# Performance work log

Measured on AMD Instinct MI355X. Metric: run time of the kernel, lower is better.

Reference implementation:

```python
import jax, jax.numpy as jnp
import numpy as np

B, F, H, D, K = 16384, 4096, 512, 64, 512  # batch, feat, hidden, emb_dim, codebook size
M = H // D  # code positions per sample


def _leaky(h):
    return jnp.where(h > 0, h, 0.01 * h)


def setup_inputs() -> dict:
    key = jax.random.key(0)
    ks = jax.random.split(key, 16)
    lin = lambda k, i, o: jax.random.normal(k, (i, o), jnp.float32) * (1.0 / np.sqrt(i))
    return {
        "x": jax.random.uniform(ks[0], (B, F), jnp.float32),
        "We1": lin(ks[1], F, 256), "be1": jnp.zeros((256,), jnp.float32),
        "We2": lin(ks[2], 256, 128), "be2": jnp.zeros((128,), jnp.float32),
        "We3": lin(ks[3], 128, H), "be3": jnp.zeros((H,), jnp.float32),
        "Wd1": lin(ks[4], H, 128), "bd1": jnp.zeros((128,), jnp.float32),
        "Wd2": lin(ks[5], 128, 256), "bd2": jnp.zeros((256,), jnp.float32),
        "Wd3": lin(ks[6], 256, F), "bd3": jnp.zeros((F,), jnp.float32),
        "codebook": jax.random.normal(ks[7], (D, K), jnp.float32) * 0.02,  # (emb_dim, num_embeddings)
    }


def _nearest(z_e, codebook):
    # z_e: (B, D, M); codebook: (D, K). Squared-distance argmin over K.
    x2 = jnp.sum(z_e * z_e, axis=1)                       # (B, M)
    xw = jnp.einsum('bdm,dk->bmk', z_e, codebook)         # (B, M, K)
    w2 = jnp.sum(codebook * codebook, axis=0)             # (K,)
    idx = jnp.argmin(x2[..., None] - 2.0 * xw + w2, axis=-1)  # (B, M)
    quant = jnp.swapaxes(codebook.T[idx], 1, 2)           # (B, D, M)
    return quant, idx


def reference(x, We1, be1, We2, be2, We3, be3, Wd1, bd1, Wd2, bd2, Wd3, bd3, codebook):
    # encoder MLP
    h = _leaky(x @ We1 + be1)
    h = _leaky(h @ We2 + be2)
    h = _leaky(h @ We3 + be3)                             # (B, H)
    z_e = h.reshape(B, D, M)
    # emb(z_e, weight_sg=True): straight-through, weight detached
    quant_sg, idx = _nearest(z_e, jax.lax.stop_gradient(codebook))
    z_q = z_e + jax.lax.stop_gradient(quant_sg - z_e)
    # emb(z_e.detach()): grads (if any) flow to codebook via gather
    emb, _ = _nearest(jax.lax.stop_gradient(z_e), codebook)
    # decoder MLP
    g = _leaky(z_q.reshape(B, H) @ Wd1 + bd1)
    g = _leaky(g @ Wd2 + bd2)
    X_pred = jax.nn.sigmoid(g @ Wd3 + bd3)                # (B, F)
    return idx, z_e, z_q, emb, X_pred
```

## Files before the change

### kernel.cpp

```cpp
#include <hip/hip_runtime.h>
#include <cstdint>
#include <cstddef>


static constexpr int BB = 16384;
static constexpr int TM = 128, TN = 128, TK = 16;

typedef __attribute__((ext_vector_type(8))) short short8;
typedef __attribute__((ext_vector_type(8))) _Float16 half8;
typedef __attribute__((ext_vector_type(4))) float f32x4;

__device__ __forceinline__ unsigned short f2bf(float f) {
    union { float f; uint32_t u; } v; v.f = f;
    uint32_t r = (v.u + 0x7FFFu + ((v.u >> 16) & 1u)) >> 16;
    return (unsigned short)r;
}

__device__ __forceinline__ int bsw(int c) { return c + ((c >> 5) << 2); }

#define GLL16(gp, lp) \
    __builtin_amdgcn_global_load_lds( \
        (const __attribute__((address_space(1))) uint32_t*)(gp), \
        (__attribute__((address_space(3))) uint32_t*)(lp), 16, 0, 0)

__global__ __launch_bounds__(256) void gemm_fp32(
    const float* __restrict__ A, const float* __restrict__ Bm,
    const float* __restrict__ bias, float* __restrict__ C,
    float* __restrict__ part,
    int M, int N, int Kd, int kLen, int act)
{
    __shared__ float As[TK][TM + 4];
    __shared__ float Bs[TK][140];
    const int tid = threadIdx.x;
    const int bm = blockIdx.y * TM;
    const int bn = blockIdx.x * TN;
    const int kStart = blockIdx.z * kLen;
    const int tx = tid & 15;
    const int ty = tid >> 4;

    const int arow = tid >> 2;
    const int acol = (tid & 3) << 2;
    const int brow = tid >> 5;
    const int bcol = (tid & 31) << 2;

    float acc[8][8];
#pragma unroll
    for (int i = 0; i < 8; i++)
#pragma unroll
        for (int j = 0; j < 8; j++) acc[i][j] = 0.f;

    const float* Ap0 = A + (size_t)(bm + arow) * Kd + acol;
    const float* Ap1 = A + (size_t)(bm + arow + 64) * Kd + acol;
    const float* Bp0 = Bm + (size_t)brow * N + bn + bcol;
    const float* Bp1 = Bm + (size_t)(brow + 8) * N + bn + bcol;

    const int pb0 = bsw(bcol);
    const int prb0 = bsw(tx * 8);
    const int prb1 = prb0 + 4;

    for (int k0 = kStart; k0 < kStart + kLen; k0 += TK) {
        const float4 a0 = *(const float4*)(Ap0 + k0);
        const float4 a1 = *(const float4*)(Ap1 + k0);
        const float4 b0 = *(const float4*)(Bp0 + (size_t)k0 * N);
        const float4 b1 = *(const float4*)(Bp1 + (size_t)k0 * N);
        __syncthreads();
        As[acol + 0][arow] = a0.x; As[acol + 1][arow] = a0.y;
        As[acol + 2][arow] = a0.z; As[acol + 3][arow] = a0.w;
        As[acol + 0][arow + 64] = a1.x; As[acol + 1][arow + 64] = a1.y;
        As[acol + 2][arow + 64] = a1.z; As[acol + 3][arow + 64] = a1.w;
        *(float4*)&Bs[brow][pb0]     = b0;
        *(float4*)&Bs[brow + 8][pb0] = b1;
        __syncthreads();
#pragma unroll
        for (int kk = 0; kk < TK; kk++) {
            float a[8], b[8];
            *(float4*)&a[0] = *(const float4*)&As[kk][ty * 8];
            *(float4*)&a[4] = *(const float4*)&As[kk][ty * 8 + 4];
            *(float4*)&b[0] = *(const float4*)&Bs[kk][prb0];
            *(float4*)&b[4] = *(const float4*)&Bs[kk][prb1];
#pragma unroll
            for (int i = 0; i < 8; i++)
#pragma unroll
                for (int j = 0; j < 8; j++)
                    acc[i][j] = fmaf(a[i], b[j], acc[i][j]);
        }
    }

    if (part) {
        float* P = part + (size_t)blockIdx.z * M * N;
#pragma unroll
        for (int i = 0; i < 8; i++) {
            const int row = bm + ty * 8 + i;
            *(float4*)&P[(size_t)row * N + bn + tx * 8]     = *(float4*)&acc[i][0];
            *(float4*)&P[(size_t)row * N + bn + tx * 8 + 4] = *(float4*)&acc[i][4];
        }
        return;
    }

    float bv[8];
#pragma unroll
    for (int j = 0; j < 8; j++) bv[j] = bias[bn + tx * 8 + j];
#pragma unroll
    for (int i = 0; i < 8; i++) {
        const int row = bm + ty * 8 + i;
        float o[8];
#pragma unroll
        for (int j = 0; j < 8; j++) {
            float v = acc[i][j] + bv[j];
            if (act == 0) v = (v > 0.f) ? v : 0.01f * v;
            else          v = 1.0f / (1.0f + __expf(-v));
            o[j] = v;
        }
        *(float4*)&C[(size_t)row * N + bn + tx * 8]     = *(float4*)&o[0];
        *(float4*)&C[(size_t)row * N + bn + tx * 8 + 4] = *(float4*)&o[4];
    }
}

__global__ __launch_bounds__(256) void combine_act(
    const float* __restrict__ part, int S, size_t MN,
    const float* __restrict__ bias, int N,
    float* __restrict__ outF, unsigned short* __restrict__ outB)
{
    const size_t e = ((size_t)blockIdx.x * 256 + threadIdx.x) * 4;
    if (e >= MN) return;
    float4 s = *(const float4*)(part + e);
    for (int i = 1; i < S; i++) {
        const float4 p = *(const float4*)(part + (size_t)i * MN + e);
        s.x += p.x; s.y += p.y; s.z += p.z; s.w += p.w;
    }
    const int col = (int)(e & (size_t)(N - 1));
    const float4 bv = *(const float4*)(bias + col);
    float v0 = s.x + bv.x, v1 = s.y + bv.y, v2 = s.z + bv.z, v3 = s.w + bv.w;
    v0 = (v0 > 0.f) ? v0 : 0.01f * v0;
    v1 = (v1 > 0.f) ? v1 : 0.01f * v1;
    v2 = (v2 > 0.f) ? v2 : 0.01f * v2;
    v3 = (v3 > 0.f) ? v3 : 0.01f * v3;
    if (outF) {
        float4 o; o.x = v0; o.y = v1; o.z = v2; o.w = v3;
        *(float4*)(outF + e) = o;
    } else {
        ushort4 o; o.x = f2bf(v0); o.y = f2bf(v1); o.z = f2bf(v2); o.w = f2bf(v3);
        *(ushort4*)(outB + e) = o;
    }
}

__global__ __launch_bounds__(256) void transpose_cast(
    const float* __restrict__ W, unsigned short* __restrict__ WT, int R, int Cc)
{
    __shared__ float s[32][33];
    const int tx = threadIdx.x & 31, ty = threadIdx.x >> 5;
    const int c0 = blockIdx.x * 32, r0 = blockIdx.y * 32;
#pragma unroll
    for (int i = 0; i < 4; i++)
        s[ty + i * 8][tx] = W[(size_t)(r0 + ty + i * 8) * Cc + c0 + tx];
    __syncthreads();
#pragma unroll
    for (int i = 0; i < 4; i++)
        WT[(size_t)(c0 + ty + i * 8) * R + r0 + tx] = f2bf(s[tx][ty + i * 8]);
}

__global__ __launch_bounds__(256) void transpose_split_f16(
    const float* __restrict__ W, unsigned short* __restrict__ Th,
    unsigned short* __restrict__ Tl, int R, int Cc)
{
    __shared__ float s[32][33];
    const int tx = threadIdx.x & 31, ty = threadIdx.x >> 5;
    const int c0 = blockIdx.x * 32, r0 = blockIdx.y * 32;
#pragma unroll
    for (int i = 0; i < 4; i++)
        s[ty + i * 8][tx] = W[(size_t)(r0 + ty + i * 8) * Cc + c0 + tx];
    __syncthreads();
#pragma unroll
    for (int i = 0; i < 4; i++) {
        const float f = s[tx][ty + i * 8];
        const _Float16 h = (_Float16)f;
        const float fh = (float)h;
        const _Float16 lo = (_Float16)((f - fh) * 4096.0f);
        union { _Float16 hf; unsigned short u; } ch, cl;
        ch.hf = h; cl.hf = lo;
        Th[(size_t)(c0 + ty + i * 8) * R + r0 + tx] = ch.u;
        Tl[(size_t)(c0 + ty + i * 8) * R + r0 + tx] = cl.u;
    }
}

__global__ __launch_bounds__(256, 2) void gemm_f16x2_enc1(
    const float* __restrict__ X,
    const unsigned short* __restrict__ Bh,
    const unsigned short* __restrict__ Bl,
    float* __restrict__ part)
{
    __shared__ short Ah[2][2048];
    __shared__ short Al[2][2048];
    const int tid = threadIdx.x;
    const int l = tid & 63, w = tid >> 6;
    const int lm = l & 15, lq = l >> 4;
    const int bm = blockIdx.y * 64;
    const int kStart = blockIdx.z * 2048;

    const float* gA = X + (size_t)(bm + w * 16 + lm) * 4096 + kStart + lq * 8;
    const unsigned short* gBh = Bh + (size_t)(w * 64 + lm) * 4096 + kStart + lq * 8;
    const unsigned short* gBl = Bl + (size_t)(w * 64 + lm) * 4096 + kStart + lq * 8;
    const size_t rstep = (size_t)16 * 4096;

    const int aoff = (w << 9) + (l << 3);
    const int fr0 = (lq << 7) + (lm << 3);

    f32x4 acc1[4][4], acc2[4][4];
#pragma unroll
    for (int i = 0; i < 4; i++)
#pragma unroll
        for (int j = 0; j < 4; j++) {
            acc1[i][j] = (f32x4){0.f, 0.f, 0.f, 0.f};
            acc2[i][j] = (f32x4){0.f, 0.f, 0.f, 0.f};
        }

    {
        float fv[8];
        *(f32x4*)&fv[0] = __builtin_nontemporal_load((const f32x4*)(gA));
        *(f32x4*)&fv[4] = __builtin_nontemporal_load((const f32x4*)(gA + 4));
        union { _Float16 h[8]; short8 s; } uh, ul;
#pragma unroll
        for (int e = 0; e < 8; e++) {
            const float f = fv[e];
            const _Float16 h = (_Float16)f;
            const float fh = (float)h;
            uh.h[e] = h;
            ul.h[e] = (_Float16)((f - fh) * 4096.0f);
        }
        *(short8*)&Ah[0][aoff] = uh.s;
        *(short8*)&Al[0][aoff] = ul.s;
    }

    for (int k0 = 0; k0 < 2048; k0 += 32) {
        const int buf = (k0 >> 5) & 1;
        const int nb = buf ^ 1;
        const int kn = k0 + 32;
        __syncthreads();
        half8 bh[4], bl[4];
#pragma unroll
        for (int j = 0; j < 4; j++) {
            bh[j] = *(const half8*)(gBh + (size_t)j * rstep + k0);
            bl[j] = *(const half8*)(gBl + (size_t)j * rstep + k0);
        }
        f32x4 a0, a1;
        if (kn < 2048) {
            a0 = __builtin_nontemporal_load((const f32x4*)(gA + kn));
            a1 = __builtin_nontemporal_load((const f32x4*)(gA + kn + 4));
        }
        half8 ah[4];
#pragma unroll
        for (int i = 0; i < 4; i++)
            ah[i] = *(const half8*)&Ah[buf][(i << 9) + fr0];
#pragma unroll
        for (int i = 0; i < 4; i++)
#pragma unroll
            for (int j = 0; j < 4; j++)
                acc1[i][j] = __builtin_amdgcn_mfma_f32_16x16x32_f16(
                    ah[i], bh[j], acc1[i][j], 0, 0, 0);
#pragma unroll
        for (int i = 0; i < 4; i++)
#pragma unroll
            for (int j = 0; j < 4; j++)
                acc2[i][j] = __builtin_amdgcn_mfma_f32_16x16x32_f16(
                    ah[i], bl[j], acc2[i][j], 0, 0, 0);
        half8 al[4];
#pragma unroll
        for (int i = 0; i < 4; i++)
            al[i] = *(const half8*)&Al[buf][(i << 9) + fr0];
#pragma unroll
        for (int i = 0; i < 4; i++)
#pragma unroll
            for (int j = 0; j < 4; j++)
                acc2[i][j] = __builtin_amdgcn_mfma_f32_16x16x32_f16(
                    al[i], bh[j], acc2[i][j], 0, 0, 0);
        if (kn < 2048) {
            float fv[8];
            *(f32x4*)&fv[0] = a0;
            *(f32x4*)&fv[4] = a1;
            union { _Float16 h[8]; short8 s; } uh, ul;
#pragma unroll
            for (int e = 0; e < 8; e++) {
                const float f = fv[e];
                const _Float16 h = (_Float16)f;
                const float fh = (float)h;
                uh.h[e] = h;
                ul.h[e] = (_Float16)((f - fh) * 4096.0f);
            }
            *(short8*)&Ah[nb][aoff] = uh.s;
            *(short8*)&Al[nb][aoff] = ul.s;
        }
    }

    float* P = part + (size_t)blockIdx.z * BB * 256;
    const float inv = 0.000244140625f;
#pragma unroll
    for (int i = 0; i < 4; i++)
#pragma unroll
        for (int j = 0; j < 4; j++) {
            const int col = w * 64 + j * 16 + lm;
#pragma unroll
            for (int r = 0; r < 4; r++) {
                const int row = bm + i * 16 + lq * 4 + r;
                P[(size_t)row * 256 + col] = acc1[i][j][r] + inv * acc2[i][j][r];
            }
        }
}

__global__ __launch_bounds__(256) void gemm_bf16_dec3(
    const unsigned short* __restrict__ Ag,
    const unsigned short* __restrict__ Bt,
    const float* __restrict__ bias, float* __restrict__ C)
{
    __shared__ short As[4096];
    __shared__ short Bs2[4096];
    const int tid = threadIdx.x;
    const int l = tid & 63, w = tid >> 6;
    const int lm = l & 15, lq = l >> 4;
    const int bm = blockIdx.y * 128, bn = blockIdx.x * 128;
    const int wm = (w >> 1) * 64, wn = (w & 1) * 64;

    const int t0 = w * 2, t1 = w * 2 + 1;
    const unsigned short* ga0 = Ag + (size_t)(bm + t0 * 16 + lm) * 256 + lq * 8;
    const unsigned short* ga1 = Ag + (size_t)(bm + t1 * 16 + lm) * 256 + lq * 8;
    const unsigned short* gb0 = Bt + (size_t)(bn + t0 * 16 + lm) * 256 + lq * 8;
    const unsigned short* gb1 = Bt + (size_t)(bn + t1 * 16 + lm) * 256 + lq * 8;

    f32x4 acc[4][4];
#pragma unroll
    for (int i = 0; i < 4; i++)
#pragma unroll
        for (int j = 0; j < 4; j++) acc[i][j] = (f32x4){0.f, 0.f, 0.f, 0.f};

    for (int k0 = 0; k0 < 256; k0 += 32) {
        __syncthreads();
        GLL16(ga0 + k0, &As[t0 * 512]);
        GLL16(ga1 + k0, &As[t1 * 512]);
        GLL16(gb0 + k0, &Bs2[t0 * 512]);
        GLL16(gb1 + k0, &Bs2[t1 * 512]);
        __syncthreads();
        short8 af[4], bf[4];
#pragma unroll
        for (int i = 0; i < 4; i++)
            af[i] = *(const short8*)&As[((w >> 1) * 4 + i) * 512 + lq * 128 + lm * 8];
#pragma unroll
        for (int j = 0; j < 4; j++)
            bf[j] = *(const short8*)&Bs2[((w & 1) * 4 + j) * 512 + lq * 128 + lm * 8];
#pragma unroll
        for (int i = 0; i < 4; i++)
#pragma unroll
            for (int j = 0; j < 4; j++)
                acc[i][j] = __builtin_amdgcn_mfma_f32_16x16x32_bf16(
                    af[i], bf[j], acc[i][j], 0, 0, 0);
    }

#pragma unroll
    for (int i = 0; i < 4; i++) {
#pragma unroll
        for (int j = 0; j < 4; j++) {
            const int col = bn + wn + j * 16 + lm;
            const float bv = bias[col];
#pragma unroll
            for (int r = 0; r < 4; r++) {
                const int row = bm + wm + i * 16 + lq * 4 + r;
                float v = acc[i][j][r] + bv;
                v = 1.0f / (1.0f + __expf(-v));
                C[(size_t)row * 4096 + col] = v;
            }
        }
    }
}

__global__ __launch_bounds__(512) void vq_argmin(
    const float* __restrict__ ze, const float* __restrict__ cb,
    float* __restrict__ idxf)
{
    __shared__ float cbs[64 * 512];
    __shared__ float As[64][68];
    __shared__ float w2s[512];
    const int tid = threadIdx.x;
    const int p0 = blockIdx.x * 64;

    const float4* cb4 = (const float4*)cb;
    float4* cbs4 = (float4*)cbs;
    for (int i = tid; i < 8192; i += 512) cbs4[i] = cb4[i];

    const float4* ze4 = (const float4*)(ze + (size_t)p0 * 64);
    for (int i = tid; i < 1024; i += 512) {
        float4 v = ze4[i];
        int e = i * 4;
        int bo = e >> 9, r = e & 511;
        int d = r >> 3, m = r & 7;
        *(float4*)&As[d][bo * 8 + m] = v;
    }
    __syncthreads();

    {
        float s = 0.f;
#pragma unroll
        for (int d = 0; d < 64; ++d) { float c = cbs[d * 512 + tid]; s = fmaf(c, c, s); }
        w2s[tid] = s;
    }
    __syncthreads();

    const int tx = tid & 63;
    const int ty = tid >> 6;

    float acc[8][8], x2a[8];
#pragma unroll
    for (int i = 0; i < 8; i++) {
        x2a[i] = 0.f;
#pragma unroll
        for (int j = 0; j < 8; j++) acc[i][j] = 0.f;
    }

#pragma unroll 8
    for (int kk = 0; kk < 64; ++kk) {
        float a[8], b[8];
        *(float4*)&a[0] = *(const float4*)&As[kk][ty * 8];
        *(float4*)&a[4] = *(const float4*)&As[kk][ty * 8 + 4];
        *(float4*)&b[0] = *(const float4*)&cbs[kk * 512 + tx * 8];
        *(float4*)&b[4] = *(const float4*)&cbs[kk * 512 + tx * 8 + 4];
#pragma unroll
        for (int i = 0; i < 8; i++) x2a[i] = fmaf(a[i], a[i], x2a[i]);
#pragma unroll
        for (int i = 0; i < 8; i++)
#pragma unroll
            for (int j = 0; j < 8; j++)
                acc[i][j] = fmaf(a[i], b[j], acc[i][j]);
    }

    float w2v[8];
#pragma unroll
    for (int j = 0; j < 8; j++) w2v[j] = w2s[tx * 8 + j];

#pragma unroll
    for (int i = 0; i < 8; i++) {
        float bd = 3.4e38f; int bk = 1 << 30;
#pragma unroll
        for (int j = 0; j < 8; j++) {
            float dsc = (x2a[i] - 2.0f * acc[i][j]) + w2v[j];
            if (dsc < bd) { bd = dsc; bk = tx * 8 + j; }
        }
        for (int off = 32; off > 0; off >>= 1) {
            float od = __shfl_xor(bd, off);
            int   ok = __shfl_xor(bk, off);
            if (od < bd || (od == bd && ok < bk)) { bd = od; bk = ok; }
        }
        if (tx == i) idxf[p0 + ty * 8 + i] = (float)bk;
    }
}

__global__ __launch_bounds__(256) void vq_gather(
    const float* __restrict__ ze, const float* __restrict__ idxf,
    const float* __restrict__ cb,
    float* __restrict__ zq, float* __restrict__ emb)
{
    const int t = blockIdx.x * 256 + threadIdx.x;
    const int e = t * 4;
    const int b = e >> 9, r = e & 511;
    const int d = r >> 3, m = r & 7;
    const float4 z = *(const float4*)(ze + e);
    float q[4];
#pragma unroll
    for (int c = 0; c < 4; c++) {
        int k = (int)idxf[b * 8 + m + c];
        q[c] = cb[d * 512 + k];
    }
    float4 zq4, em4;
    zq4.x = z.x + (q[0] - z.x); zq4.y = z.y + (q[1] - z.y);
    zq4.z = z.z + (q[2] - z.z); zq4.w = z.w + (q[3] - z.w);
    em4.x = q[0]; em4.y = q[1]; em4.z = q[2]; em4.w = q[3];
    *(float4*)(zq + e) = zq4;
    *(float4*)(emb + e) = em4;
}

extern "C" void kernel_launch(void* const* d_in, const int* in_sizes, int n_in,
                              void* d_out, int out_size, void* d_ws, size_t ws_size,
                              hipStream_t stream)
{
    const float* x   = (const float*)d_in[0];
    const float* We1 = (const float*)d_in[1];
    const float* be1 = (const float*)d_in[2];
    const float* We2 = (const float*)d_in[3];
    const float* be2 = (const float*)d_in[4];
    const float* We3 = (const float*)d_in[5];
    const float* be3 = (const float*)d_in[6];
    const float* Wd1 = (const float*)d_in[7];
    const float* bd1 = (const float*)d_in[8];
    const float* Wd2 = (const float*)d_in[9];
    const float* bd2 = (const float*)d_in[10];
    const float* Wd3 = (const float*)d_in[11];
    const float* bd3 = (const float*)d_in[12];
    const float* cb  = (const float*)d_in[13];

    float* out   = (float*)d_out;
    float* o_idx = out;
    float* o_ze  = o_idx + 131072;
    float* o_zq  = o_ze + 8388608;
    float* o_emb = o_zq + 8388608;
    float* o_X   = o_emb + 8388608;

    float* h1 = (float*)d_ws;
    float* h2 = h1 + (size_t)BB * 256;
    float* g1 = h1;
    unsigned short* g2b = (unsigned short*)(h1 + (size_t)BB * 128);
    unsigned short* WT  = (unsigned short*)h2;

    unsigned short* Bth = (unsigned short*)(o_X + 16777216);
    unsigned short* Btl = Bth + 1048576;

    transpose_split_f16<<<dim3(8, 128), 256, 0, stream>>>(We1, Bth, Btl, 4096, 256);
    gemm_f16x2_enc1<<<dim3(1, 256, 2), 256, 0, stream>>>(x, Bth, Btl, o_X);
    combine_act<<<4096, 256, 0, stream>>>(o_X, 2, (size_t)BB * 256, be1, 256, h1, nullptr);
    gemm_fp32<<<dim3(1, 128, 2), 256, 0, stream>>>(
        h1, We2, nullptr, nullptr, o_X, BB, 128, 256, 128, 0);
    combine_act<<<2048, 256, 0, stream>>>(o_X, 2, (size_t)BB * 128, be2, 128, h2, nullptr);
    gemm_fp32<<<dim3(4, 128, 1), 256, 0, stream>>>(
        h2, We3, be3, o_ze, nullptr, BB, 512, 128, 128, 0);

    vq_argmin<<<dim3(2048), dim3(512), 0, stream>>>(o_ze, cb, o_idx);
    vq_gather<<<dim3(8192), dim3(256), 0, stream>>>(o_ze, o_idx, cb, o_zq, o_emb);

    transpose_cast<<<dim3(128, 8), 256, 0, stream>>>(Wd3, WT, 256, 4096);

    gemm_fp32<<<dim3(1, 128, 4), 256, 0, stream>>>(
        o_zq, Wd1, nullptr, nullptr, o_X, BB, 128, 512, 128, 0);
    combine_act<<<2048, 256, 0, stream>>>(o_X, 4, (size_t)BB * 128, bd1, 128, g1, nullptr);
    gemm_fp32<<<dim3(2, 128, 2), 256, 0, stream>>>(
        g1, Wd2, nullptr, nullptr, o_X, BB, 256, 128, 64, 0);
    combine_act<<<4096, 256, 0, stream>>>(o_X, 2, (size_t)BB * 256, bd2, 256, nullptr, g2b);
    gemm_bf16_dec3<<<dim3(32, 128), 256, 0, stream>>>(g2b, WT, bd3, o_X);
}
```

Baseline: 1.080 ms.

## Deepen software pipeline in enc1 GEMM with register-prefetched B-high and two-ahead A loads

Restructures the first encoder GEMM's main loop into a templated step, unrolled by two. The B-high fragments for the next k-step are prefetched into ping-pong registers and the fp32 A tile is loaded two steps ahead, so global load latency is hidden behind more MFMA work. The cost is more live registers (an extra B buffer and the A prefetch), which may pressure the 2-blocks-per-CU launch bound or cause spills.

```diff
diff --git a/kernel.cpp b/kernel.cpp
--- a/kernel.cpp
+++ b/kernel.cpp
@@ -183,6 +183,79 @@
     }
 }
 
+template<int BUF>
+__device__ __forceinline__ void enc1_step(
+    int K0,
+    const float* __restrict__ gA,
+    const unsigned short* __restrict__ gBh,
+    const unsigned short* __restrict__ gBl,
+    short (&Ah)[2][2048], short (&Al)[2][2048],
+    half8 (&bhC)[4], half8 (&bhN)[4], half8 (&blS)[4],
+    f32x4& p0, f32x4& p1,
+    f32x4 (&acc1)[4][4], f32x4 (&acc2)[4][4],
+    int aoff, int fr0)
+{
+    constexpr size_t rstep = (size_t)16 * 4096;
+    const int kn1 = K0 + 32, kn2 = K0 + 64;
+    __syncthreads();
+#pragma unroll
+    for (int j = 0; j < 4; j++)
+        blS[j] = *(const half8*)(gBl + (size_t)j * rstep + K0);
+    if (kn1 < 2048) {
+#pragma unroll
+        for (int j = 0; j < 4; j++)
+            bhN[j] = *(const half8*)(gBh + (size_t)j * rstep + kn1);
+    }
+    f32x4 f0, f1;
+    if (kn2 < 2048) {
+        f0 = __builtin_nontemporal_load((const f32x4*)(gA + kn2));
+        f1 = __builtin_nontemporal_load((const f32x4*)(gA + kn2 + 4));
+    }
+    half8 ah[4];
+#pragma unroll
+    for (int i = 0; i < 4; i++)
+        ah[i] = *(const half8*)&Ah[BUF][(i << 9) + fr0];
+#pragma unroll
+    for (int i = 0; i < 4; i++)
+#pragma unroll
+        for (int j = 0; j < 4; j++)
+            acc1[i][j] = __builtin_amdgcn_mfma_f32_16x16x32_f16(
+                ah[i], bhC[j], acc1[i][j], 0, 0, 0);
+#pragma unroll
+    for (int i = 0; i < 4; i++)
+#pragma unroll
+        for (int j = 0; j < 4; j++)
+            acc2[i][j] = __builtin_amdgcn_mfma_f32_16x16x32_f16(
+                ah[i], blS[j], acc2[i][j], 0, 0, 0);
+    half8 al[4];
+#pragma unroll
+    for (int i = 0; i < 4; i++)
+        al[i] = *(const half8*)&Al[BUF][(i << 9) + fr0];
+#pragma unroll
+    for (int i = 0; i < 4; i++)
+#pragma unroll
+        for (int j = 0; j < 4; j++)
+            acc2[i][j] = __builtin_amdgcn_mfma_f32_16x16x32_f16(
+                al[i], bhC[j], acc2[i][j], 0, 0, 0);
+    if (kn1 < 2048) {
+        float fv[8];
+        *(f32x4*)&fv[0] = p0;
+        *(f32x4*)&fv[4] = p1;
+        union { _Float16 h[8]; short8 s; } uh, ul;
+#pragma unroll
+        for (int e = 0; e < 8; e++) {
+            const float f = fv[e];
+            const _Float16 h = (_Float16)f;
+            const float fh = (float)h;
+            uh.h[e] = h;
+            ul.h[e] = (_Float16)((f - fh) * 4096.0f);
+        }
+        *(short8*)&Ah[BUF ^ 1][aoff] = uh.s;
+        *(short8*)&Al[BUF ^ 1][aoff] = ul.s;
+    }
+    if (kn2 < 2048) { p0 = f0; p1 = f1; }
+}
+
 __global__ __launch_bounds__(256, 2) void gemm_f16x2_enc1(
     const float* __restrict__ X,
     const unsigned short* __restrict__ Bh,
@@ -200,7 +273,7 @@
     const float* gA = X + (size_t)(bm + w * 16 + lm) * 4096 + kStart + lq * 8;
     const unsigned short* gBh = Bh + (size_t)(w * 64 + lm) * 4096 + kStart + lq * 8;
     const unsigned short* gBl = Bl + (size_t)(w * 64 + lm) * 4096 + kStart + lq * 8;
-    const size_t rstep = (size_t)16 * 4096;
+    constexpr size_t rstep = (size_t)16 * 4096;
 
     const int aoff = (w << 9) + (l << 3);
     const int fr0 = (lq << 7) + (lm << 3);
@@ -214,10 +287,20 @@
             acc2[i][j] = (f32x4){0.f, 0.f, 0.f, 0.f};
         }
 
+    half8 bhA[4], bhB[4], blS[4];
+    f32x4 p0, p1;
+
     {
+#pragma unroll
+        for (int j = 0; j < 4; j++)
+            bhA[j] = *(const half8*)(gBh + (size_t)j * rstep);
+        f32x4 a0 = __builtin_nontemporal_load((const f32x4*)(gA));
+        f32x4 a1 = __builtin_nontemporal_load((const f32x4*)(gA + 4));
+        p0 = __builtin_nontemporal_load((const f32x4*)(gA + 32));
+        p1 = __builtin_nontemporal_load((const f32x4*)(gA + 36));
         float fv[8];
-        *(f32x4*)&fv[0] = __builtin_nontemporal_load((const f32x4*)(gA));
-        *(f32x4*)&fv[4] = __builtin_nontemporal_load((const f32x4*)(gA + 4));
+        *(f32x4*)&fv[0] = a0;
+        *(f32x4*)&fv[4] = a1;
         union { _Float16 h[8]; short8 s; } uh, ul;
 #pragma unroll
         for (int e = 0; e < 8; e++) {
@@ -231,64 +314,11 @@
         *(short8*)&Al[0][aoff] = ul.s;
     }
 
-    for (int k0 = 0; k0 < 2048; k0 += 32) {
-        const int buf = (k0 >> 5) & 1;
-        const int nb = buf ^ 1;
-        const int kn = k0 + 32;
-        __syncthreads();
-        half8 bh[4], bl[4];
-#pragma unroll
-        for (int j = 0; j < 4; j++) {
-            bh[j] = *(const half8*)(gBh + (size_t)j * rstep + k0);
-            bl[j] = *(const half8*)(gBl + (size_t)j * rstep + k0);
-        }
-        f32x4 a0, a1;
-        if (kn < 2048) {
-            a0 = __builtin_nontemporal_load((const f32x4*)(gA + kn));
-            a1 = __builtin_nontemporal_load((const f32x4*)(gA + kn + 4));
-        }
-        half8 ah[4];
-#pragma unroll
-        for (int i = 0; i < 4; i++)
-            ah[i] = *(const half8*)&Ah[buf][(i << 9) + fr0];
-#pragma unroll
-        for (int i = 0; i < 4; i++)
-#pragma unroll
-            for (int j = 0; j < 4; j++)
-                acc1[i][j] = __builtin_amdgcn_mfma_f32_16x16x32_f16(
-                    ah[i], bh[j], acc1[i][j], 0, 0, 0);
-#pragma unroll
-        for (int i = 0; i < 4; i++)
-#pragma unroll
-            for (int j = 0; j < 4; j++)
-                acc2[i][j] = __builtin_amdgcn_mfma_f32_16x16x32_f16(
-                    ah[i], bl[j], acc2[i][j], 0, 0, 0);
-        half8 al[4];
-#pragma unroll
-        for (int i = 0; i < 4; i++)
-            al[i] = *(const half8*)&Al[buf][(i << 9) + fr0];
-#pragma unroll
-        for (int i = 0; i < 4; i++)
-#pragma unroll
-            for (int j = 0; j < 4; j++)
-                acc2[i][j] = __builtin_amdgcn_mfma_f32_16x16x32_f16(
-                    al[i], bh[j], acc2[i][j], 0, 0, 0);
-        if (kn < 2048) {
-            float fv[8];
-            *(f32x4*)&fv[0] = a0;
-            *(f32x4*)&fv[4] = a1;
-            union { _Float16 h[8]; short8 s; } uh, ul;
-#pragma unroll
-            for (int e = 0; e < 8; e++) {
-                const float f = fv[e];
-                const _Float16 h = (_Float16)f;
-                const float fh = (float)h;
-                uh.h[e] = h;
-                ul.h[e] = (_Float16)((f - fh) * 4096.0f);
-            }
-            *(short8*)&Ah[nb][aoff] = uh.s;
-            *(short8*)&Al[nb][aoff] = ul.s;
-        }
+    for (int k2 = 0; k2 < 2048; k2 += 64) {
+        enc1_step<0>(k2,      gA, gBh, gBl, Ah, Al, bhA, bhB, blS,
+                     p0, p1, acc1, acc2, aoff, fr0);
+        enc1_step<1>(k2 + 32, gA, gBh, gBl, Ah, Al, bhB, bhA, blS,
+                     p0, p1, acc1, acc2, aoff, fr0);
     }
 
     float* P = part + (size_t)blockIdx.z * BB * 256;
```

New measurement: 1.056 ms. 1.02x faster.
